# Performance work log

Hardware: AMD Instinct MI355X
Metric: run time of the kernel (lower is better)

Reference implementation:

```python
import jax, jax.numpy as jnp
import numpy as np

B, N, D = 1, 4301, 768          # batch, tokens (4200 patch + 1 cls + 100 det), dim
H, HD = 12, 64                  # heads, head_dim (all_head_dim = 768)
NDET = 100                      # det tokens at the end of the sequence
EPS = 1e-5                      # torch LayerNorm default eps
SCALE = HD ** -0.5


def setup_inputs() -> dict:
    key = jax.random.key(0)
    ks = jax.random.split(key, 10)
    w = lambda k: jax.random.normal(k, (D, D), dtype=jnp.float32) * 0.02
    return {
        "x": jax.random.normal(ks[0], (B, N, D), dtype=jnp.float32),
        "wq_p": w(ks[1]), "wk_p": w(ks[2]), "wv_p": w(ks[3]),
        "wq_d": w(ks[4]), "wk_d": w(ks[5]), "wv_d": w(ks[6]),
        "bq_p": jnp.zeros((D,), jnp.float32), "bv_p": jnp.zeros((D,), jnp.float32),
        "bq_d": jnp.zeros((D,), jnp.float32), "bv_d": jnp.zeros((D,), jnp.float32),
        "ln_g": jnp.ones((D,), jnp.float32), "ln_b": jnp.zeros((D,), jnp.float32),
        "wo_p": w(ks[7]), "bo_p": jnp.zeros((D,), jnp.float32),
        "wo_d": w(ks[8]), "bo_d": jnp.zeros((D,), jnp.float32),
    }


def reference(x, wq_p, wk_p, wv_p, wq_d, wk_d, wv_d,
              bq_p, bv_p, bq_d, bv_d, ln_g, ln_b,
              wo_p, bo_p, wo_d, bo_d):
    xp = x[:, :-NDET, :]                       # [B, N-100, D] patch (+cls) tokens
    xd = x[:, -NDET:, :]                       # [B, 100, D]   det tokens
    # separate patch/det QKV projections (subln=True path; k has no bias)
    q = jnp.concatenate([xp @ wq_p.T + bq_p, xd @ wq_d.T + bq_d], axis=1)
    k = jnp.concatenate([xp @ wk_p.T,        xd @ wk_d.T],        axis=1)
    v = jnp.concatenate([xp @ wv_p.T + bv_p, xd @ wv_d.T + bv_d], axis=1)
    split = lambda t: t.reshape(B, N, H, HD).transpose(0, 2, 1, 3)  # [B,H,N,HD]
    q, k, v = split(q) * SCALE, split(k), split(v)
    # unfused attention (memory_efficient_attention_pytorch, attn_mask=None)
    attn = jax.nn.softmax(jnp.einsum("bhqd,bhkd->bhqk", q, k), axis=-1)
    o = jnp.einsum("bhqk,bhkd->bhqd", attn, v)
    o = o.transpose(0, 2, 1, 3).reshape(B, N, D)
    # inner_attn_ln (LayerNorm over all_head_dim)
    mu = o.mean(-1, keepdims=True)
    var = ((o - mu) ** 2).mean(-1, keepdims=True)
    o = (o - mu) * jax.lax.rsqrt(var + EPS) * ln_g + ln_b
    # separate patch/det output projections
    out = jnp.concatenate([o[:, :-NDET, :] @ wo_p.T + bo_p,
                           o[:, -NDET:, :] @ wo_d.T + bo_d], axis=1)
    return out
```

## Files before the change

kernel.cpp:

```cpp
#include <hip/hip_runtime.h>
#include <hip/hip_bf16.h>

#define NT 4301
#define NP 4201
#define NDET 100
#define DMODEL 768
#define NHEAD 12
#define HD 64
#define LN_EPS 1e-5f
#define LOG2E 1.4426950408889634f
#define QSCALE (0.125f * LOG2E)
#define NTP 4352
#define NCHUNK 68
#define FRAGSZ 512
#define CHUNKSZ 4096

typedef __hip_bfloat16 bf16;
typedef __attribute__((ext_vector_type(4))) float f32x4;
typedef __attribute__((ext_vector_type(8))) short frag8;
typedef __attribute__((ext_vector_type(2))) unsigned int u32x2;

static __device__ __forceinline__ void permlane32_swap(unsigned& a, unsigned& b) {
#if __has_builtin(__builtin_amdgcn_permlane32_swap)
    u32x2 r = __builtin_amdgcn_permlane32_swap(a, b, false, false);
    a = r[0]; b = r[1];
#else
    asm("v_permlane32_swap_b32 %0, %1" : "+v"(a), "+v"(b));
#endif
}
static __device__ __forceinline__ void permlane16_swap(unsigned& a, unsigned& b) {
#if __has_builtin(__builtin_amdgcn_permlane16_swap)
    u32x2 r = __builtin_amdgcn_permlane16_swap(a, b, false, false);
    a = r[0]; b = r[1];
#else
    asm("v_permlane16_swap_b32 %0, %1" : "+v"(a), "+v"(b));
#endif
}

static __device__ __forceinline__ float fast_exp2(float x) {
#if __has_builtin(__builtin_amdgcn_exp2f)
    return __builtin_amdgcn_exp2f(x);
#else
    return __builtin_exp2f(x);
#endif
}

static __device__ __forceinline__ unsigned pack_bf16_tr(float a, float b) {
    return __builtin_amdgcn_perm(__builtin_bit_cast(unsigned, b),
                                 __builtin_bit_cast(unsigned, a), 0x07060302u);
}

static __device__ __forceinline__ void gload16(const bf16* g, bf16* l) {
    __builtin_amdgcn_global_load_lds(
        (const __attribute__((address_space(1))) void*)g,
        (__attribute__((address_space(3))) void*)l, 16, 0, 0);
}

__global__ __launch_bounds__(256) void cast_all_kernel(
    const float* __restrict__ x,
    const float* __restrict__ w0, const float* __restrict__ w1,
    const float* __restrict__ w2, const float* __restrict__ w3,
    const float* __restrict__ w4, const float* __restrict__ w5,
    const float* __restrict__ w6, const float* __restrict__ w7,
    bf16* __restrict__ dst, int nx, int nw, int total) {
    int i4 = (blockIdx.x * 256 + threadIdx.x) * 4;
    if (i4 >= total) return;
    const float* s;
    int off;
    if (i4 < nx) {
        s = x; off = i4;
    } else {
        int r = i4 - nx;
        int w = r / nw;
        off = r - w * nw;
        s = w0;
        if (w == 1) s = w1; else if (w == 2) s = w2; else if (w == 3) s = w3;
        else if (w == 4) s = w4; else if (w == 5) s = w5;
        else if (w == 6) s = w6; else if (w == 7) s = w7;
    }
    float4 v = *(const float4*)(s + off);
    bf16 o[4] = {__float2bfloat16(v.x), __float2bfloat16(v.y),
                 __float2bfloat16(v.z), __float2bfloat16(v.w)};
    *(ushort4*)(dst + i4) = *(ushort4*)o;
}

__global__ __launch_bounds__(256, 4) void qkv_kernel(
    const bf16* __restrict__ xb, const bf16* __restrict__ wbase,
    const float* __restrict__ bq_p, const float* __restrict__ bq_d,
    const float* __restrict__ bv_p, const float* __restrict__ bv_d,
    bf16* __restrict__ Qb, bf16* __restrict__ Ksw, bf16* __restrict__ Vsw) {
    __shared__ bf16 As[2][64][32];
    __shared__ bf16 Bs[2][192][32];

    const int tid = threadIdx.x;
    const int wave = tid >> 6, lane = tid & 63;
    const int quad = lane >> 4, l16 = lane & 15;
    const int bx = blockIdx.x;
    const int h = blockIdx.y;
    const int is_det = bx >= 66;
    const int row0 = is_det ? NP + (bx - 66) * 64 : bx * 64;
    const int Mlim = is_det ? NT : NP;
    const int col0 = h * 64;
    const size_t nw = (size_t)DMODEL * DMODEL;
    const bf16* W = wbase + (is_det ? 3 * nw : 0);

    const f32x4 z4 = {0.f, 0.f, 0.f, 0.f};
    f32x4 acc[4][3];
#pragma unroll
    for (int r4 = 0; r4 < 4; ++r4)
#pragma unroll
        for (int f = 0; f < 3; ++f) acc[r4][f] = z4;

    const int srow = tid >> 2;
    const int scol8 = (tid & 3) * 8;
    int a_r = row0 + srow;
    if (a_r >= Mlim) a_r = Mlim - 1;
    const bf16* ap = xb + (size_t)a_r * DMODEL + scol8;
    const bf16* bp = W + (size_t)(col0 + srow) * DMODEL + scol8;

    bf16* asb[2] = {&As[0][0][0] + wave * 512, &As[1][0][0] + wave * 512};
    bf16* bsb[2] = {&Bs[0][0][0] + wave * 512, &Bs[1][0][0] + wave * 512};

    {
        gload16(ap, asb[0]);
        gload16(bp, bsb[0]);
        gload16(bp + nw, bsb[0] + 2048);
        gload16(bp + 2 * nw, bsb[0] + 4096);
    }
    __asm__ volatile("s_waitcnt vmcnt(0)" ::: "memory");
    __builtin_amdgcn_s_barrier();
    __asm__ volatile("" ::: "memory");

    int p = 0;
    for (int k0 = 0; k0 < DMODEL; k0 += 32) {
        if (k0 + 32 < DMODEL) {
            const int kn = k0 + 32;
            gload16(ap + kn, asb[p ^ 1]);
            gload16(bp + kn, bsb[p ^ 1]);
            gload16(bp + nw + kn, bsb[p ^ 1] + 2048);
            gload16(bp + 2 * nw + kn, bsb[p ^ 1] + 4096);
        }
        frag8 af[4], bfr[3];
#pragma unroll
        for (int r4 = 0; r4 < 4; ++r4)
            af[r4] = *(const frag8*)(&As[p][r4 * 16 + l16][quad * 8]);
#pragma unroll
        for (int f = 0; f < 3; ++f)
            bfr[f] = *(const frag8*)(&Bs[p][wave * 48 + f * 16 + l16][quad * 8]);
#pragma unroll
        for (int r4 = 0; r4 < 4; ++r4)
#pragma unroll
            for (int f = 0; f < 3; ++f)
                acc[r4][f] = __builtin_amdgcn_mfma_f32_16x16x32_bf16(af[r4], bfr[f], acc[r4][f], 0, 0, 0);
        __asm__ volatile("s_waitcnt vmcnt(0)" ::: "memory");
        __builtin_amdgcn_s_barrier();
        __asm__ volatile("" ::: "memory");
        p ^= 1;
    }

#pragma unroll
    for (int f = 0; f < 3; ++f) {
        const int oc = 3 * wave + f;
        const int opi = oc >> 2;
        const int cin = (oc & 3) * 16 + l16;
        const int c = col0 + cin;
        float bv = 0.f, scale = 1.f;
        if (opi == 0) { bv = (is_det ? bq_d : bq_p)[c]; scale = QSCALE; }
        else if (opi == 2) { bv = (is_det ? bv_d : bv_p)[c]; }
#pragma unroll
        for (int r4 = 0; r4 < 4; ++r4) {
#pragma unroll
            for (int j = 0; j < 4; ++j) {
                const int r = row0 + r4 * 16 + quad * 4 + j;
                if (r >= Mlim) continue;
                const bf16 val = __float2bfloat16((acc[r4][f][j] + bv) * scale);
                if (opi == 0) {
                    Qb[(size_t)r * DMODEL + c] = val;
                } else if (opi == 1) {
                    const int cc = r >> 6, tf = (r >> 4) & 3, ln = r & 15;
                    const int s = cin >> 5, qd = (cin >> 3) & 3, je = cin & 7;
                    Ksw[((size_t)(h * NCHUNK + cc) * 8 + tf * 2 + s) * FRAGSZ +
                        (qd * 16 + ln) * 8 + je] = val;
                } else {
                    const int t = cin >> 4, le = cin & 15;
                    const int cc = r >> 6, rr = r & 63;
                    const int sv = rr >> 5, qv = (rr >> 3) & 3, je = rr & 7;
                    Vsw[((size_t)(h * NCHUNK + cc) * 8 + t * 2 + sv) * FRAGSZ +
                        (qv * 16 + le) * 8 + je] = val;
                }
            }
        }
    }
}

__global__ __launch_bounds__(256, 4) void attn_kernel(
    const bf16* __restrict__ Q, const bf16* __restrict__ Ksw,
    const bf16* __restrict__ Vsw, float* __restrict__ O_part,
    float* __restrict__ l_part, int cpb) {
    __shared__ bf16 KV[2][16][FRAGSZ];

    const int tid = threadIdx.x;
    const int wave = tid >> 6, lane = tid & 63;
    const int quad = lane >> 4, l16 = lane & 15;

    int bx, h, z;
    {
        const int id = blockIdx.x;
        const int nblk = gridDim.x;
        const int per = nblk >> 3;
        if ((nblk & 7) == 0 && per % 34 == 0) {
            const int ppx = per / 34;
            const int q = id >> 3;
            const int pair = (id & 7) * ppx + q / 34;
            bx = q % 34;
            h = pair % NHEAD; z = pair / NHEAD;
        } else {
            bx = id % 34; h = (id / 34) % NHEAD; z = id / (34 * NHEAD);
        }
    }
    const int qbase = bx * 128;
    const int hoff = h * HD;
    const int c0 = z * cpb, c1 = c0 + cpb;

    frag8 ones;
#pragma unroll
    for (int j = 0; j < 8; ++j) ones[j] = (short)0x3F80;

    frag8 qf[2][2];
#pragma unroll
    for (int g = 0; g < 2; ++g) {
        int qr = qbase + wave * 32 + g * 16 + l16;
        if (qr >= NT) qr = NT - 1;
#pragma unroll
        for (int s = 0; s < 2; ++s)
            qf[g][s] = *(const frag8*)(Q + (size_t)qr * DMODEL + hoff + s * 32 + quad * 8);
    }

    const bf16* kb0 = Ksw + (size_t)h * NCHUNK * CHUNKSZ + lane * 8;
    const bf16* vb0 = Vsw + (size_t)h * NCHUNK * CHUNKSZ + lane * 8;
    const bf16* sb = (wave < 2) ? kb0 : vb0;
    const int foff = (wave & 1) * 4;
    const int fbase = 4 * wave;

    const f32x4 z4 = {0.f, 0.f, 0.f, 0.f};
    f32x4 accO[2][4], accL[2];
#pragma unroll
    for (int g = 0; g < 2; ++g) {
        accL[g] = z4;
#pragma unroll
        for (int t = 0; t < 4; ++t) accO[g][t] = z4;
    }

    {
        const bf16* s = sb + (size_t)c0 * CHUNKSZ + foff * FRAGSZ;
#pragma unroll
        for (int i = 0; i < 4; ++i)
            gload16(s + i * FRAGSZ, &KV[0][fbase + i][0]);
    }
    __asm__ volatile("s_waitcnt vmcnt(0)" ::: "memory");
    __builtin_amdgcn_s_barrier();
    __asm__ volatile("" ::: "memory");

    int p = 0;
    for (int c = c0; c < c1; ++c) {
        if (c + 1 < c1) {
            const bf16* s = sb + (size_t)(c + 1) * CHUNKSZ + foff * FRAGSZ;
#pragma unroll
            for (int i = 0; i < 4; ++i)
                gload16(s + i * FRAGSZ, &KV[p ^ 1][fbase + i][0]);
        }

        f32x4 S[2][4];
#pragma unroll
        for (int t = 0; t < 4; ++t) {
            const frag8 k0 = *(const frag8*)(&KV[p][t * 2 + 0][lane * 8]);
            const frag8 k1 = *(const frag8*)(&KV[p][t * 2 + 1][lane * 8]);
#pragma unroll
            for (int g = 0; g < 2; ++g) {
                f32x4 s0 = __builtin_amdgcn_mfma_f32_16x16x32_bf16(k0, qf[g][0], z4, 0, 0, 0);
                S[g][t]  = __builtin_amdgcn_mfma_f32_16x16x32_bf16(k1, qf[g][1], s0, 0, 0, 0);
            }
        }
        if (c == NCHUNK - 1) {
            const int kb = c * 64 + quad * 4;
#pragma unroll
            for (int t = 0; t < 4; ++t)
#pragma unroll
                for (int j = 0; j < 4; ++j)
                    if (kb + t * 16 + j >= NT) {
                        S[0][t][j] = -1e30f;
                        S[1][t][j] = -1e30f;
                    }
        }

        frag8 pf[2][2];
#pragma unroll
        for (int g = 0; g < 2; ++g) {
            unsigned lo[4], hi[4];
#pragma unroll
            for (int t = 0; t < 4; ++t) {
                lo[t] = pack_bf16_tr(fast_exp2(S[g][t][0]), fast_exp2(S[g][t][1]));
                hi[t] = pack_bf16_tr(fast_exp2(S[g][t][2]), fast_exp2(S[g][t][3]));
            }
#pragma unroll
            for (int s = 0; s < 2; ++s) {
                unsigned A = lo[2 * s], B = hi[2 * s];
                unsigned C = lo[2 * s + 1], D = hi[2 * s + 1];
                permlane32_swap(A, C);
                permlane32_swap(B, D);
                permlane16_swap(A, C);
                permlane16_swap(B, D);
                union { unsigned u[4]; frag8 f; } pu;
                pu.u[0] = A; pu.u[1] = B; pu.u[2] = C; pu.u[3] = D;
                pf[g][s] = pu.f;
                accL[g] = __builtin_amdgcn_mfma_f32_16x16x32_bf16(pf[g][s], ones, accL[g], 0, 0, 0);
            }
        }

#pragma unroll
        for (int s = 0; s < 2; ++s)
#pragma unroll
            for (int t = 0; t < 4; ++t) {
                const frag8 v = *(const frag8*)(&KV[p][8 + t * 2 + s][lane * 8]);
#pragma unroll
                for (int g = 0; g < 2; ++g)
                    accO[g][t] = __builtin_amdgcn_mfma_f32_16x16x32_bf16(pf[g][s], v, accO[g][t], 0, 0, 0);
            }

        __asm__ volatile("s_waitcnt vmcnt(0)" ::: "memory");
        __builtin_amdgcn_s_barrier();
        __asm__ volatile("" ::: "memory");
        p ^= 1;
    }

    float* Op = O_part + (size_t)z * NT * DMODEL;
#pragma unroll
    for (int g = 0; g < 2; ++g)
#pragma unroll
        for (int j = 0; j < 4; ++j) {
            const int r = qbase + wave * 32 + g * 16 + quad * 4 + j;
            if (r < NT) {
#pragma unroll
                for (int t = 0; t < 4; ++t)
                    Op[(size_t)r * DMODEL + hoff + t * 16 + l16] = accO[g][t][j];
                if (l16 == 0)
                    l_part[((size_t)z * NHEAD + h) * NTP + r] = accL[g][j];
            }
        }
}

__global__ __launch_bounds__(192) void reduce_ln_kernel(
    const float* __restrict__ O_part, const float* __restrict__ l_part,
    const float* __restrict__ g, const float* __restrict__ b,
    bf16* __restrict__ out, int nsplit) {
    const int n = blockIdx.x;
    const int tid = threadIdx.x;
    const int d0 = tid * 4;
    const int hh = d0 >> 6;

    float4 o = make_float4(0.f, 0.f, 0.f, 0.f);
    float lv = 0.f;
    for (int s = 0; s < nsplit; ++s) {
        float4 v = *(const float4*)(O_part + ((size_t)s * NT + n) * DMODEL + d0);
        o.x += v.x; o.y += v.y; o.z += v.z; o.w += v.w;
        lv += l_part[((size_t)s * NHEAD + hh) * NTP + n];
    }
    const float inv_l = 1.0f / lv;
    float vals[4] = {o.x * inv_l, o.y * inv_l, o.z * inv_l, o.w * inv_l};

    float s = vals[0] + vals[1] + vals[2] + vals[3];
    float s2 = vals[0] * vals[0] + vals[1] * vals[1] + vals[2] * vals[2] + vals[3] * vals[3];
#pragma unroll
    for (int off = 1; off < 64; off <<= 1) {
        s += __shfl_xor(s, off);
        s2 += __shfl_xor(s2, off);
    }
    __shared__ float ss[3], ss2[3];
    const int wave = tid >> 6, lane = tid & 63;
    if (lane == 0) { ss[wave] = s; ss2[wave] = s2; }
    __syncthreads();
    s = ss[0] + ss[1] + ss[2];
    s2 = ss2[0] + ss2[1] + ss2[2];
    const float mu = s * (1.0f / 768.0f);
    float var = s2 * (1.0f / 768.0f) - mu * mu;
    const float inv = rsqrtf(var + LN_EPS);

    unsigned short pk[4];
#pragma unroll
    for (int i = 0; i < 4; ++i) {
        const int d = d0 + i;
        const float v = (vals[i] - mu) * inv * g[d] + b[d];
        bf16 bb = __float2bfloat16(v);
        pk[i] = *(unsigned short*)&bb;
    }
    *(ushort4*)(out + (size_t)n * DMODEL + d0) = *(ushort4*)pk;
}

__global__ __launch_bounds__(256, 4) void out_kernel(
    const bf16* __restrict__ Lb, const bf16* __restrict__ wo,
    const float* __restrict__ bo_p, const float* __restrict__ bo_d,
    float* __restrict__ out) {
    __shared__ bf16 As[128][32];
    __shared__ bf16 Bs[64][32];

    const int tid = threadIdx.x;
    const int wave = tid >> 6, lane = tid & 63;
    const int quad = lane >> 4, l16 = lane & 15;
    const int bx = blockIdx.x;
    const int is_det = bx >= 33;
    const int row0 = is_det ? NP : bx * 128;
    const int Mlim = is_det ? NT : NP;
    const int col0 = blockIdx.y * 64;
    const size_t nw = (size_t)DMODEL * DMODEL;
    const bf16* B = wo + (is_det ? nw : 0);
    const float* bias = is_det ? bo_d : bo_p;

    const f32x4 z4 = {0.f, 0.f, 0.f, 0.f};
    f32x4 acc[2][4];
#pragma unroll
    for (int gg = 0; gg < 2; ++gg)
#pragma unroll
        for (int t = 0; t < 4; ++t) acc[gg][t] = z4;

    const int arow = tid >> 1;
    const int acol = (tid & 1) * 16;
    int a_r = row0 + arow;
    if (a_r >= Mlim) a_r = Mlim - 1;
    const bf16* ap = Lb + (size_t)a_r * DMODEL + acol;
    const int brow = tid >> 2;
    const int bcol = (tid & 3) * 8;
    const bf16* bp = B + (size_t)(col0 + brow) * DMODEL + bcol;

    uint4 areg0 = *(const uint4*)(ap);
    uint4 areg1 = *(const uint4*)(ap + 8);
    uint4 breg  = *(const uint4*)(bp);

    for (int k0 = 0; k0 < DMODEL; k0 += 32) {
        __syncthreads();
        *(uint4*)(&As[arow][acol]) = areg0;
        *(uint4*)(&As[arow][acol + 8]) = areg1;
        *(uint4*)(&Bs[brow][bcol]) = breg;
        if (k0 + 32 < DMODEL) {
            areg0 = *(const uint4*)(ap + k0 + 32);
            areg1 = *(const uint4*)(ap + k0 + 40);
            breg  = *(const uint4*)(bp + k0 + 32);
        }
        __asm__ volatile("s_waitcnt lgkmcnt(0)" ::: "memory");
        __builtin_amdgcn_s_barrier();
        __asm__ volatile("" ::: "memory");
        frag8 af[2], bfq[4];
#pragma unroll
        for (int gg = 0; gg < 2; ++gg)
            af[gg] = *(const frag8*)(&As[wave * 32 + gg * 16 + l16][quad * 8]);
#pragma unroll
        for (int t = 0; t < 4; ++t)
            bfq[t] = *(const frag8*)(&Bs[t * 16 + l16][quad * 8]);
#pragma unroll
        for (int gg = 0; gg < 2; ++gg)
#pragma unroll
            for (int t = 0; t < 4; ++t)
                acc[gg][t] = __builtin_amdgcn_mfma_f32_16x16x32_bf16(af[gg], bfq[t], acc[gg][t], 0, 0, 0);
        __asm__ volatile("" ::: "memory");
    }

#pragma unroll
    for (int gg = 0; gg < 2; ++gg) {
        const int rbase = row0 + wave * 32 + gg * 16 + quad * 4;
#pragma unroll
        for (int t = 0; t < 4; ++t) {
            const int c = col0 + t * 16 + l16;
            const float bv = bias[c];
#pragma unroll
            for (int j = 0; j < 4; ++j) {
                const int r = rbase + j;
                if (r < Mlim) out[(size_t)r * DMODEL + c] = acc[gg][t][j] + bv;
            }
        }
    }
}

extern "C" void kernel_launch(void* const* d_in, const int* in_sizes, int n_in,
                              void* d_out, int out_size, void* d_ws, size_t ws_size,
                              hipStream_t stream) {
    const float* x    = (const float*)d_in[0];
    const float* wq_p = (const float*)d_in[1];
    const float* wk_p = (const float*)d_in[2];
    const float* wv_p = (const float*)d_in[3];
    const float* wq_d = (const float*)d_in[4];
    const float* wk_d = (const float*)d_in[5];
    const float* wv_d = (const float*)d_in[6];
    const float* bq_p = (const float*)d_in[7];
    const float* bv_p = (const float*)d_in[8];
    const float* bq_d = (const float*)d_in[9];
    const float* bv_d = (const float*)d_in[10];
    const float* ln_g = (const float*)d_in[11];
    const float* ln_b = (const float*)d_in[12];
    const float* wo_p = (const float*)d_in[13];
    const float* bo_p = (const float*)d_in[14];
    const float* wo_d = (const float*)d_in[15];
    const float* bo_d = (const float*)d_in[16];
    float* out = (float*)d_out;

    const size_t nx  = (size_t)NT * DMODEL;
    const size_t nsw = (size_t)NHEAD * NCHUNK * CHUNKSZ;
    const size_t nw  = (size_t)DMODEL * DMODEL;

    char* ws = (char*)d_ws;
    bf16* xb   = (bf16*)ws; ws += nx * 2;
    bf16* wqkv = (bf16*)ws; ws += 6 * nw * 2;
    bf16* wob  = (bf16*)ws; ws += 2 * nw * 2;
    bf16* Qb   = (bf16*)ws; ws += nx * 2;
    bf16* Ksw  = (bf16*)ws; ws += nsw * 2;
    bf16* Vsw  = (bf16*)ws; ws += nsw * 2;
    const size_t fixed = (size_t)(ws - (char*)d_ws);

    const size_t per_split = nx * 4 + (size_t)NHEAD * NTP * 4;
    int nsplit = 1;
    if (ws_size >= fixed + 4 * per_split) nsplit = 4;
    else if (ws_size >= fixed + 2 * per_split) nsplit = 2;
    const int cpb = NCHUNK / nsplit;

    float* O_part = (float*)ws;
    float* l_part = (float*)(ws + (size_t)nsplit * nx * 4);
    bf16* Lb = xb;

    const int total = (int)(nx + 8 * nw);
    cast_all_kernel<<<dim3((total / 4 + 255) / 256), dim3(256), 0, stream>>>(
        x, wq_p, wk_p, wv_p, wq_d, wk_d, wv_d, wo_p, wo_d, xb, (int)nx, (int)nw, total);

    qkv_kernel<<<dim3(68, 12), dim3(256), 0, stream>>>(
        xb, wqkv, bq_p, bq_d, bv_p, bv_d, Qb, Ksw, Vsw);

    attn_kernel<<<dim3(34 * NHEAD * nsplit), dim3(256), 0, stream>>>(
        Qb, Ksw, Vsw, O_part, l_part, cpb);

    reduce_ln_kernel<<<dim3(NT), dim3(192), 0, stream>>>(
        O_part, l_part, ln_g, ln_b, Lb, nsplit);

    out_kernel<<<dim3(34, 12), dim3(256), 0, stream>>>(Lb, wob, bo_p, bo_d, out);
}
```

Baseline: 229.9 us.

## Double-buffer out-projection GEMM with direct global-to-LDS loads; cap attention split at two

The output-projection GEMM now uses two LDS buffers and fills them with direct global-to-LDS loads (gload16), prefetching the next K-tile while the current one feeds the MFMAs. This drops the register staging and the LDS store step and leaves one barrier per iteration. Separately, the attention split-K factor is capped at 2 instead of 4. That halves the partial-output traffic and reduction work but gives the attention kernel fewer blocks to run in parallel.

```diff
diff --git a/kernel.cpp b/kernel.cpp
--- a/kernel.cpp
+++ b/kernel.cpp
@@ -400,8 +400,8 @@
     const bf16* __restrict__ Lb, const bf16* __restrict__ wo,
     const float* __restrict__ bo_p, const float* __restrict__ bo_d,
     float* __restrict__ out) {
-    __shared__ bf16 As[128][32];
-    __shared__ bf16 Bs[64][32];
+    __shared__ bf16 As[2][128][32];
+    __shared__ bf16 Bs[2][64][32];
 
     const int tid = threadIdx.x;
     const int wave = tid >> 6, lane = tid & 63;
@@ -422,45 +422,50 @@
 #pragma unroll
         for (int t = 0; t < 4; ++t) acc[gg][t] = z4;
 
-    const int arow = tid >> 1;
-    const int acol = (tid & 1) * 16;
-    int a_r = row0 + arow;
-    if (a_r >= Mlim) a_r = Mlim - 1;
-    const bf16* ap = Lb + (size_t)a_r * DMODEL + acol;
-    const int brow = tid >> 2;
-    const int bcol = (tid & 3) * 8;
-    const bf16* bp = B + (size_t)(col0 + brow) * DMODEL + bcol;
-
-    uint4 areg0 = *(const uint4*)(ap);
-    uint4 areg1 = *(const uint4*)(ap + 8);
-    uint4 breg  = *(const uint4*)(bp);
-
+    const int sr = tid >> 2;
+    const int sc = (tid & 3) * 8;
+    int ar0 = row0 + sr;       if (ar0 >= Mlim) ar0 = Mlim - 1;
+    int ar1 = row0 + 64 + sr;  if (ar1 >= Mlim) ar1 = Mlim - 1;
+    const bf16* ap0 = Lb + (size_t)ar0 * DMODEL + sc;
+    const bf16* ap1 = Lb + (size_t)ar1 * DMODEL + sc;
+    const bf16* bp  = B + (size_t)(col0 + sr) * DMODEL + sc;
+
+    bf16* asb[2] = {&As[0][0][0] + wave * 512, &As[1][0][0] + wave * 512};
+    bf16* bsb[2] = {&Bs[0][0][0] + wave * 512, &Bs[1][0][0] + wave * 512};
+
+    {
+        gload16(ap0, asb[0]);
+        gload16(ap1, asb[0] + 2048);
+        gload16(bp,  bsb[0]);
+    }
+    __asm__ volatile("s_waitcnt vmcnt(0)" ::: "memory");
+    __builtin_amdgcn_s_barrier();
+    __asm__ volatile("" ::: "memory");
+
+    int p = 0;
     for (int k0 = 0; k0 < DMODEL; k0 += 32) {
-        __syncthreads();
-        *(uint4*)(&As[arow][acol]) = areg0;
-        *(uint4*)(&As[arow][acol + 8]) = areg1;
-        *(uint4*)(&Bs[brow][bcol]) = breg;
         if (k0 + 32 < DMODEL) {
-            areg0 = *(const uint4*)(ap + k0 + 32);
-            areg1 = *(const uint4*)(ap + k0 + 40);
-            breg  = *(const uint4*)(bp + k0 + 32);
-        }
-        __asm__ volatile("s_waitcnt lgkmcnt(0)" ::: "memory");
+            const int kn = k0 + 32;
+            gload16(ap0 + kn, asb[p ^ 1]);
+            gload16(ap1 + kn, asb[p ^ 1] + 2048);
+            gload16(bp + kn,  bsb[p ^ 1]);
+        }
+        frag8 af[2], bfq[4];
+#pragma unroll
+        for (int gg = 0; gg < 2; ++gg)
+            af[gg] = *(const frag8*)(&As[p][wave * 32 + gg * 16 + l16][quad * 8]);
+#pragma unroll
+        for (int t = 0; t < 4; ++t)
+            bfq[t] = *(const frag8*)(&Bs[p][t * 16 + l16][quad * 8]);
+#pragma unroll
+        for (int gg = 0; gg < 2; ++gg)
+#pragma unroll
+            for (int t = 0; t < 4; ++t)
+                acc[gg][t] = __builtin_amdgcn_mfma_f32_16x16x32_bf16(af[gg], bfq[t], acc[gg][t], 0, 0, 0);
+        __asm__ volatile("s_waitcnt vmcnt(0)" ::: "memory");
         __builtin_amdgcn_s_barrier();
         __asm__ volatile("" ::: "memory");
-        frag8 af[2], bfq[4];
-#pragma unroll
-        for (int gg = 0; gg < 2; ++gg)
-            af[gg] = *(const frag8*)(&As[wave * 32 + gg * 16 + l16][quad * 8]);
-#pragma unroll
-        for (int t = 0; t < 4; ++t)
-            bfq[t] = *(const frag8*)(&Bs[t * 16 + l16][quad * 8]);
-#pragma unroll
-        for (int gg = 0; gg < 2; ++gg)
-#pragma unroll
-            for (int t = 0; t < 4; ++t)
-                acc[gg][t] = __builtin_amdgcn_mfma_f32_16x16x32_bf16(af[gg], bfq[t], acc[gg][t], 0, 0, 0);
-        __asm__ volatile("" ::: "memory");
+        p ^= 1;
     }
 
 #pragma unroll
@@ -516,8 +521,7 @@
 
     const size_t per_split = nx * 4 + (size_t)NHEAD * NTP * 4;
     int nsplit = 1;
-    if (ws_size >= fixed + 4 * per_split) nsplit = 4;
-    else if (ws_size >= fixed + 2 * per_split) nsplit = 2;
+    if (ws_size >= fixed + 2 * per_split) nsplit = 2;
     const int cpb = NCHUNK / nsplit;
 
     float* O_part = (float*)ws;
```

Result: no change. 232.8 us (+1.3%).
